# Performance work log

Hardware: AMD Instinct MI355X
Metric: run time of the kernel (lower is better)

The kernel has to match this reference:

```python
import jax, jax.numpy as jnp
import numpy as np

N_IN = 128
N_BASIS = 16


def setup_inputs() -> dict:
    key = jax.random.key(0)
    ks = jax.random.split(key, 6)
    N, P = 50000, 200000
    prop = jax.random.normal(ks[0], (N, N_IN), dtype=jnp.float32)
    idx_i = jax.random.randint(ks[1], (P,), 0, N, dtype=jnp.int64)
    idx_j = jax.random.randint(ks[2], (P,), 0, N, dtype=jnp.int64)
    basis = jax.random.normal(ks[3], (P, N_BASIS), dtype=jnp.float32)
    # bias-free MLP: n_in=128 -> hidden 256 (tanh) -> n_out=2048
    W1 = jax.random.normal(ks[4], (N_IN, 256), dtype=jnp.float32) * (1.0 / np.sqrt(N_IN))
    W2 = jax.random.normal(ks[5], (256, N_IN * N_BASIS), dtype=jnp.float32) * (1.0 / np.sqrt(256))
    return {"prop": prop, "idx_i": idx_i, "idx_j": idx_j, "basis": basis, "W1": W1, "W2": W2}


def reference(prop, idx_i, idx_j, basis, W1, W2):
    # gather node features at edge endpoints and sum
    inter = prop[idx_i] + prop[idx_j]              # [P, n_in]
    # bias-free MLP with tanh on hidden layer
    h = jnp.tanh(inter @ W1)                       # [P, 256]
    h = h @ W2                                     # [P, n_in * n_basis]
    # contract with per-edge basis: 'pcb,pb->pc'
    h = h.reshape(-1, N_IN, N_BASIS)               # [P, n_in, n_basis]
    out = jnp.einsum('pcb,pb->pc', h, basis)       # [P, n_in]
    return out[:, None, :]                         # [P, 1, n_in]
```

## Files before the change

### kernel.cpp

```cpp
#include <hip/hip_runtime.h>

#define N_IN 128
#define HID 256
#define NB 16
#define BM 128
#define HS_STRIDE 264
#define BS_STRIDE 17

typedef __attribute__((ext_vector_type(8))) short s8v;
typedef __attribute__((ext_vector_type(4))) float f4v;

__device__ __forceinline__ unsigned short f2bf(float f) {
  unsigned int u = __float_as_uint(f);
  u += 0x7fffu + ((u >> 16) & 1u);
  return (unsigned short)(u >> 16);
}

__device__ __forceinline__ float tanh_fast(float x) {
  float e = __expf(2.0f * x);
  return 1.0f - 2.0f * __builtin_amdgcn_rcpf(e + 1.0f);
}

__global__ void prep_kernel(const float* __restrict__ W1, const float* __restrict__ W2,
                            unsigned short* __restrict__ W1f, unsigned short* __restrict__ W2f) {
  int tid = blockIdx.x * blockDim.x + threadIdx.x;
  if (tid < N_IN * HID) {
    int j = tid & 7, lane = (tid >> 3) & 63, ct = (tid >> 9) & 7, kk = (tid >> 12) & 3, pass = tid >> 14;
    int n = pass * 128 + ct * 16 + (lane & 15);
    int k = kk * 32 + (lane >> 4) * 8 + j;
    W1f[tid] = f2bf(W1[k * HID + n]);
  }
  int i = tid - N_IN * HID;
  if (i >= 0 && i < HID * (N_IN * NB)) {
    int j = i & 7, lane = (i >> 3) & 63, ct = (i >> 9) & 7, kk = (i >> 12) & 7, b = i >> 15;
    int n = ct * 16 + (lane & 15);
    int k = kk * 32 + (lane >> 4) * 8 + j;
    W2f[i] = f2bf(W2[k * (N_IN * NB) + n * 16 + b]);
  }
}

__global__ void __launch_bounds__(256, 2)
pilayer_kernel(const float* __restrict__ prop,
               const int* __restrict__ idx_i,
               const int* __restrict__ idx_j,
               const float* __restrict__ basis,
               const unsigned short* __restrict__ W1f,
               const unsigned short* __restrict__ W2f,
               float* __restrict__ out, int P) {
  __shared__ unsigned short Hs[BM * HS_STRIDE];
  __shared__ float basisS[BM * BS_STRIDE];

  const int t = threadIdx.x;
  const int lane = t & 63;
  const int wv = t >> 6;
  const int l15 = lane & 15;
  const int l4 = lane >> 4;
  const int tile0 = blockIdx.x * BM;
  const int row0 = wv * 32;

  int pidx[2], qidx[2];
#pragma unroll
  for (int rt = 0; rt < 2; ++rt) {
    int p = tile0 + row0 + rt * 16 + l15; if (p >= P) p = P - 1;
    pidx[rt] = idx_i[p];
    qidx[rt] = idx_j[p];
  }

  {
    int r = t >> 1;
    int c0 = (t & 1) * 8;
    int p = tile0 + r; if (p >= P) p = P - 1;
    const f4v* bp = (const f4v*)(basis + (long)p * NB + c0);
    f4v b0 = __builtin_nontemporal_load(bp);
    f4v b1 = __builtin_nontemporal_load(bp + 1);
    float* dst = &basisS[r * BS_STRIDE + c0];
    dst[0] = b0[0]; dst[1] = b0[1]; dst[2] = b0[2]; dst[3] = b0[3];
    dst[4] = b1[0]; dst[5] = b1[1]; dst[6] = b1[2]; dst[7] = b1[3];
  }

  {
    s8v afr[4][2];
#pragma unroll
    for (int kk = 0; kk < 4; ++kk) {
      int k0 = kk * 32 + l4 * 8;
#pragma unroll
      for (int rt = 0; rt < 2; ++rt) {
        const float4* ai = (const float4*)(prop + (long)pidx[rt] * N_IN + k0);
        const float4* aj = (const float4*)(prop + (long)qidx[rt] * N_IN + k0);
        float4 x0 = ai[0], x1 = ai[1];
        float4 y0 = aj[0], y1 = aj[1];
        s8v a;
        a[0] = (short)f2bf(x0.x + y0.x); a[1] = (short)f2bf(x0.y + y0.y);
        a[2] = (short)f2bf(x0.z + y0.z); a[3] = (short)f2bf(x0.w + y0.w);
        a[4] = (short)f2bf(x1.x + y1.x); a[5] = (short)f2bf(x1.y + y1.y);
        a[6] = (short)f2bf(x1.z + y1.z); a[7] = (short)f2bf(x1.w + y1.w);
        afr[kk][rt] = a;
      }
    }
#pragma unroll
    for (int pass = 0; pass < 2; ++pass) {
      f4v acc[2][8];
#pragma unroll
      for (int rt = 0; rt < 2; ++rt)
#pragma unroll
        for (int ct = 0; ct < 8; ++ct) acc[rt][ct] = (f4v){0.f, 0.f, 0.f, 0.f};
#pragma unroll
      for (int kk = 0; kk < 4; ++kk) {
#pragma unroll
        for (int ct = 0; ct < 8; ++ct) {
          s8v bfr = *(const s8v*)(W1f + ((((pass * 4 + kk) * 8 + ct) * 64 + lane) << 3));
#pragma unroll
          for (int rt = 0; rt < 2; ++rt)
            acc[rt][ct] = __builtin_amdgcn_mfma_f32_16x16x32_bf16(afr[kk][rt], bfr, acc[rt][ct], 0, 0, 0);
        }
      }
#pragma unroll
      for (int rt = 0; rt < 2; ++rt)
#pragma unroll
        for (int ct = 0; ct < 8; ++ct)
#pragma unroll
          for (int r = 0; r < 4; ++r) {
            int lrow = row0 + rt * 16 + l4 * 4 + r;
            int col = pass * 128 + ct * 16 + l15;
            Hs[lrow * HS_STRIDE + col] = f2bf(tanh_fast(acc[rt][ct][r]));
          }
    }
  }

  __syncthreads();

  const int rg = wv >> 1, cg = wv & 1;
  const int rbase = rg * 64;

  f4v o[4][4];
#pragma unroll
  for (int rt = 0; rt < 4; ++rt)
#pragma unroll
    for (int q = 0; q < 4; ++q) o[rt][q] = (f4v){0.f, 0.f, 0.f, 0.f};

#pragma unroll 1
  for (int khalf = 0; khalf < 2; ++khalf) {
    s8v areg[4][4];
#pragma unroll
    for (int rt = 0; rt < 4; ++rt)
#pragma unroll
      for (int kloc = 0; kloc < 4; ++kloc)
        areg[rt][kloc] = *(const s8v*)&Hs[(rbase + rt * 16 + l15) * HS_STRIDE +
                                          (khalf * 4 + kloc) * 32 + l4 * 8];

    s8v bf[4][4];
#pragma unroll
    for (int q0 = 0; q0 < 3; ++q0)
#pragma unroll
      for (int kloc = 0; kloc < 4; ++kloc)
        bf[q0][kloc] = *(const s8v*)(W2f +
            ((((khalf * 4 + kloc) * 8) + cg * 4 + q0) << 9) + lane * 8);

#pragma unroll 1
    for (int b = 0; b < 16; ++b) {
      float bs[4][4];
#pragma unroll
      for (int rt = 0; rt < 4; ++rt)
#pragma unroll
        for (int r = 0; r < 4; ++r)
          bs[rt][r] = basisS[(rbase + rt * 16 + l4 * 4 + r) * BS_STRIDE + b];

#pragma unroll
      for (int q = 0; q < 4; ++q) {
        {
          int nb = b + ((q + 3) >> 2); if (nb > 15) nb = 15;
          int nq = (q + 3) & 3;
#pragma unroll
          for (int kloc = 0; kloc < 4; ++kloc)
            bf[(q + 3) & 3][kloc] = *(const s8v*)(W2f +
                (((nb * 8 + khalf * 4 + kloc) * 8 + cg * 4 + nq) << 9) + lane * 8);
        }
        f4v g[4];
#pragma unroll
        for (int rt = 0; rt < 4; ++rt) g[rt] = (f4v){0.f, 0.f, 0.f, 0.f};
        __builtin_amdgcn_s_setprio(1);
#pragma unroll
        for (int kloc = 0; kloc < 4; ++kloc)
#pragma unroll
          for (int rt = 0; rt < 4; ++rt)
            g[rt] = __builtin_amdgcn_mfma_f32_16x16x32_bf16(areg[rt][kloc], bf[q][kloc], g[rt], 0, 0, 0);
        __builtin_amdgcn_s_setprio(0);
#pragma unroll
        for (int rt = 0; rt < 4; ++rt)
#pragma unroll
          for (int r = 0; r < 4; ++r)
            o[rt][q][r] += g[rt][r] * bs[rt][r];
      }
    }
  }

#pragma unroll
  for (int rt = 0; rt < 4; ++rt)
#pragma unroll
    for (int r = 0; r < 4; ++r) {
      int p = tile0 + rbase + rt * 16 + l4 * 4 + r;
      if (p < P) {
        float* op = out + (long)p * N_IN + cg * 64 + l15;
#pragma unroll
        for (int q = 0; q < 4; ++q)
          __builtin_nontemporal_store(o[rt][q][r], op + q * 16);
      }
    }
}

extern "C" void kernel_launch(void* const* d_in, const int* in_sizes, int n_in,
                              void* d_out, int out_size, void* d_ws, size_t ws_size,
                              hipStream_t stream) {
  const float* prop  = (const float*)d_in[0];
  const int* idx_i   = (const int*)d_in[1];
  const int* idx_j   = (const int*)d_in[2];
  const float* basis = (const float*)d_in[3];
  const float* W1    = (const float*)d_in[4];
  const float* W2    = (const float*)d_in[5];
  float* out = (float*)d_out;
  int P = in_sizes[1];

  unsigned short* W1f = (unsigned short*)d_ws;
  unsigned short* W2f = W1f + N_IN * HID;

  int prep_threads = N_IN * HID + HID * N_IN * NB;
  prep_kernel<<<(prep_threads + 255) / 256, 256, 0, stream>>>(W1, W2, W1f, W2f);

  int ntiles = (P + BM - 1) / BM;
  pilayer_kernel<<<ntiles, 256, 0, stream>>>(prop, idx_i, idx_j, basis, W1f, W2f, out, P);
}
```

Before: 338.2 us.

## Split fused kernel into hidden-layer kernel and W2/basis contraction kernel

Splits the fused kernel into two launches. The first computes the tanh hidden activations and writes them to a workspace buffer in MFMA fragment order. The second reads those fragments straight into registers, applies W2 and contracts with the basis. The aim is to free the second kernel from the large shared-memory H tile, which could allow more concurrent blocks, and to make the GEMM1 and GEMM2 phases independent. The cost is an extra global write and read of roughly 64KB per tile plus a second launch, and it falls back to the fused kernel when the workspace is too small.

```diff
diff --git a/kernel.cpp b/kernel.cpp
--- a/kernel.cpp
+++ b/kernel.cpp
@@ -39,16 +39,14 @@
   }
 }
 
+
 __global__ void __launch_bounds__(256, 2)
-pilayer_kernel(const float* __restrict__ prop,
-               const int* __restrict__ idx_i,
-               const int* __restrict__ idx_j,
-               const float* __restrict__ basis,
-               const unsigned short* __restrict__ W1f,
-               const unsigned short* __restrict__ W2f,
-               float* __restrict__ out, int P) {
+h_kernel(const float* __restrict__ prop,
+         const int* __restrict__ idx_i,
+         const int* __restrict__ idx_j,
+         const unsigned short* __restrict__ W1f,
+         unsigned short* __restrict__ Hg, int P) {
   __shared__ unsigned short Hs[BM * HS_STRIDE];
-  __shared__ float basisS[BM * BS_STRIDE];
 
   const int t = threadIdx.x;
   const int lane = t & 63;
@@ -64,18 +62,6 @@
     int p = tile0 + row0 + rt * 16 + l15; if (p >= P) p = P - 1;
     pidx[rt] = idx_i[p];
     qidx[rt] = idx_j[p];
-  }
-
-  {
-    int r = t >> 1;
-    int c0 = (t & 1) * 8;
-    int p = tile0 + r; if (p >= P) p = P - 1;
-    const f4v* bp = (const f4v*)(basis + (long)p * NB + c0);
-    f4v b0 = __builtin_nontemporal_load(bp);
-    f4v b1 = __builtin_nontemporal_load(bp + 1);
-    float* dst = &basisS[r * BS_STRIDE + c0];
-    dst[0] = b0[0]; dst[1] = b0[1]; dst[2] = b0[2]; dst[3] = b0[3];
-    dst[4] = b1[0]; dst[5] = b1[1]; dst[6] = b1[2]; dst[7] = b1[3];
   }
 
   {
@@ -129,6 +115,221 @@
 
   __syncthreads();
 
+  {
+    const int fbase = t >> 6;
+    unsigned short* base = Hg + ((long)blockIdx.x << 15);
+#pragma unroll
+    for (int fi = 0; fi < 16; ++fi) {
+      int frag = fi * 4 + fbase;
+      int rowblk = frag >> 3, kk = frag & 7;
+      int row = rowblk * 16 + l15;
+      int k0 = kk * 32 + l4 * 8;
+      s8v v = *(const s8v*)&Hs[row * HS_STRIDE + k0];
+      __builtin_nontemporal_store(v, (s8v*)(base + ((frag * 64 + lane) << 3)));
+    }
+  }
+}
+
+__global__ void __launch_bounds__(256, 2)
+c_kernel(const unsigned short* __restrict__ Hg,
+         const float* __restrict__ basis,
+         const unsigned short* __restrict__ W2f,
+         float* __restrict__ out, int P) {
+  __shared__ float basisS[BM * BS_STRIDE];
+
+  const int t = threadIdx.x;
+  const int lane = t & 63;
+  const int wv = t >> 6;
+  const int l15 = lane & 15;
+  const int l4 = lane >> 4;
+  const int tile0 = blockIdx.x * BM;
+
+  {
+    int r = t >> 1;
+    int c0 = (t & 1) * 8;
+    int p = tile0 + r; if (p >= P) p = P - 1;
+    const f4v* bp = (const f4v*)(basis + (long)p * NB + c0);
+    f4v b0 = __builtin_nontemporal_load(bp);
+    f4v b1 = __builtin_nontemporal_load(bp + 1);
+    float* dst = &basisS[r * BS_STRIDE + c0];
+    dst[0] = b0[0]; dst[1] = b0[1]; dst[2] = b0[2]; dst[3] = b0[3];
+    dst[4] = b1[0]; dst[5] = b1[1]; dst[6] = b1[2]; dst[7] = b1[3];
+  }
+
+  const int rg = wv >> 1, cg = wv & 1;
+  const int rbase = rg * 64;
+
+  __syncthreads();
+
+  f4v o[4][4];
+#pragma unroll
+  for (int rt = 0; rt < 4; ++rt)
+#pragma unroll
+    for (int q = 0; q < 4; ++q) o[rt][q] = (f4v){0.f, 0.f, 0.f, 0.f};
+
+  const unsigned short* hbase = Hg + ((long)blockIdx.x << 15);
+
+#pragma unroll 1
+  for (int khalf = 0; khalf < 2; ++khalf) {
+    s8v areg[4][4];
+#pragma unroll
+    for (int rt = 0; rt < 4; ++rt)
+#pragma unroll
+      for (int kloc = 0; kloc < 4; ++kloc) {
+        int frag = ((rg * 4 + rt) << 3) + khalf * 4 + kloc;
+        areg[rt][kloc] = *(const s8v*)(hbase + ((frag * 64 + lane) << 3));
+      }
+
+    s8v bf[4][4];
+#pragma unroll
+    for (int q0 = 0; q0 < 3; ++q0)
+#pragma unroll
+      for (int kloc = 0; kloc < 4; ++kloc)
+        bf[q0][kloc] = *(const s8v*)(W2f +
+            ((((khalf * 4 + kloc) * 8) + cg * 4 + q0) << 9) + lane * 8);
+
+#pragma unroll 1
+    for (int b = 0; b < 16; ++b) {
+      float bs[4][4];
+#pragma unroll
+      for (int rt = 0; rt < 4; ++rt)
+#pragma unroll
+        for (int r = 0; r < 4; ++r)
+          bs[rt][r] = basisS[(rbase + rt * 16 + l4 * 4 + r) * BS_STRIDE + b];
+
+#pragma unroll
+      for (int q = 0; q < 4; ++q) {
+        {
+          int nb = b + ((q + 3) >> 2); if (nb > 15) nb = 15;
+          int nq = (q + 3) & 3;
+#pragma unroll
+          for (int kloc = 0; kloc < 4; ++kloc)
+            bf[(q + 3) & 3][kloc] = *(const s8v*)(W2f +
+                (((nb * 8 + khalf * 4 + kloc) * 8 + cg * 4 + nq) << 9) + lane * 8);
+        }
+        f4v g[4];
+#pragma unroll
+        for (int rt = 0; rt < 4; ++rt) g[rt] = (f4v){0.f, 0.f, 0.f, 0.f};
+        __builtin_amdgcn_s_setprio(1);
+#pragma unroll
+        for (int kloc = 0; kloc < 4; ++kloc)
+#pragma unroll
+          for (int rt = 0; rt < 4; ++rt)
+            g[rt] = __builtin_amdgcn_mfma_f32_16x16x32_bf16(areg[rt][kloc], bf[q][kloc], g[rt], 0, 0, 0);
+        __builtin_amdgcn_s_setprio(0);
+#pragma unroll
+        for (int rt = 0; rt < 4; ++rt)
+#pragma unroll
+          for (int r = 0; r < 4; ++r)
+            o[rt][q][r] += g[rt][r] * bs[rt][r];
+      }
+    }
+  }
+
+#pragma unroll
+  for (int rt = 0; rt < 4; ++rt)
+#pragma unroll
+    for (int r = 0; r < 4; ++r) {
+      int p = tile0 + rbase + rt * 16 + l4 * 4 + r;
+      if (p < P) {
+        float* op = out + (long)p * N_IN + cg * 64 + l15;
+#pragma unroll
+        for (int q = 0; q < 4; ++q)
+          __builtin_nontemporal_store(o[rt][q][r], op + q * 16);
+      }
+    }
+}
+
+__global__ void __launch_bounds__(256, 2)
+pilayer_kernel(const float* __restrict__ prop,
+               const int* __restrict__ idx_i,
+               const int* __restrict__ idx_j,
+               const float* __restrict__ basis,
+               const unsigned short* __restrict__ W1f,
+               const unsigned short* __restrict__ W2f,
+               float* __restrict__ out, int P) {
+  __shared__ unsigned short Hs[BM * HS_STRIDE];
+  __shared__ float basisS[BM * BS_STRIDE];
+
+  const int t = threadIdx.x;
+  const int lane = t & 63;
+  const int wv = t >> 6;
+  const int l15 = lane & 15;
+  const int l4 = lane >> 4;
+  const int tile0 = blockIdx.x * BM;
+  const int row0 = wv * 32;
+
+  int pidx[2], qidx[2];
+#pragma unroll
+  for (int rt = 0; rt < 2; ++rt) {
+    int p = tile0 + row0 + rt * 16 + l15; if (p >= P) p = P - 1;
+    pidx[rt] = idx_i[p];
+    qidx[rt] = idx_j[p];
+  }
+
+  {
+    int r = t >> 1;
+    int c0 = (t & 1) * 8;
+    int p = tile0 + r; if (p >= P) p = P - 1;
+    const f4v* bp = (const f4v*)(basis + (long)p * NB + c0);
+    f4v b0 = __builtin_nontemporal_load(bp);
+    f4v b1 = __builtin_nontemporal_load(bp + 1);
+    float* dst = &basisS[r * BS_STRIDE + c0];
+    dst[0] = b0[0]; dst[1] = b0[1]; dst[2] = b0[2]; dst[3] = b0[3];
+    dst[4] = b1[0]; dst[5] = b1[1]; dst[6] = b1[2]; dst[7] = b1[3];
+  }
+
+  {
+    s8v afr[4][2];
+#pragma unroll
+    for (int kk = 0; kk < 4; ++kk) {
+      int k0 = kk * 32 + l4 * 8;
+#pragma unroll
+      for (int rt = 0; rt < 2; ++rt) {
+        const float4* ai = (const float4*)(prop + (long)pidx[rt] * N_IN + k0);
+        const float4* aj = (const float4*)(prop + (long)qidx[rt] * N_IN + k0);
+        float4 x0 = ai[0], x1 = ai[1];
+        float4 y0 = aj[0], y1 = aj[1];
+        s8v a;
+        a[0] = (short)f2bf(x0.x + y0.x); a[1] = (short)f2bf(x0.y + y0.y);
+        a[2] = (short)f2bf(x0.z + y0.z); a[3] = (short)f2bf(x0.w + y0.w);
+        a[4] = (short)f2bf(x1.x + y1.x); a[5] = (short)f2bf(x1.y + y1.y);
+        a[6] = (short)f2bf(x1.z + y1.z); a[7] = (short)f2bf(x1.w + y1.w);
+        afr[kk][rt] = a;
+      }
+    }
+#pragma unroll
+    for (int pass = 0; pass < 2; ++pass) {
+      f4v acc[2][8];
+#pragma unroll
+      for (int rt = 0; rt < 2; ++rt)
+#pragma unroll
+        for (int ct = 0; ct < 8; ++ct) acc[rt][ct] = (f4v){0.f, 0.f, 0.f, 0.f};
+#pragma unroll
+      for (int kk = 0; kk < 4; ++kk) {
+#pragma unroll
+        for (int ct = 0; ct < 8; ++ct) {
+          s8v bfr = *(const s8v*)(W1f + ((((pass * 4 + kk) * 8 + ct) * 64 + lane) << 3));
+#pragma unroll
+          for (int rt = 0; rt < 2; ++rt)
+            acc[rt][ct] = __builtin_amdgcn_mfma_f32_16x16x32_bf16(afr[kk][rt], bfr, acc[rt][ct], 0, 0, 0);
+        }
+      }
+#pragma unroll
+      for (int rt = 0; rt < 2; ++rt)
+#pragma unroll
+        for (int ct = 0; ct < 8; ++ct)
+#pragma unroll
+          for (int r = 0; r < 4; ++r) {
+            int lrow = row0 + rt * 16 + l4 * 4 + r;
+            int col = pass * 128 + ct * 16 + l15;
+            Hs[lrow * HS_STRIDE + col] = f2bf(tanh_fast(acc[rt][ct][r]));
+          }
+    }
+  }
+
+  __syncthreads();
+
   const int rg = wv >> 1, cg = wv & 1;
   const int rbase = rg * 64;
 
@@ -222,10 +423,18 @@
 
   unsigned short* W1f = (unsigned short*)d_ws;
   unsigned short* W2f = W1f + N_IN * HID;
+  unsigned short* Hg  = W2f + HID * (N_IN * NB);
 
   int prep_threads = N_IN * HID + HID * N_IN * NB;
   prep_kernel<<<(prep_threads + 255) / 256, 256, 0, stream>>>(W1, W2, W1f, W2f);
 
   int ntiles = (P + BM - 1) / BM;
-  pilayer_kernel<<<ntiles, 256, 0, stream>>>(prop, idx_i, idx_j, basis, W1f, W2f, out, P);
-}
+  size_t need = (size_t)prep_threads * 2 + (size_t)ntiles * 65536;
+
+  if (ws_size >= need) {
+    h_kernel<<<ntiles, 256, 0, stream>>>(prop, idx_i, idx_j, W1f, Hg, P);
+    c_kernel<<<ntiles, 256, 0, stream>>>(Hg, basis, W2f, out, P);
+  } else {
+    pilayer_kernel<<<ntiles, 256, 0, stream>>>(prop, idx_i, idx_j, basis, W1f, W2f, out, P);
+  }
+}
```

After: 369.7 us. +9.3%, slower.
